# Kernel tuning notes

Measured on AMD Instinct MI355X. Metric: run time of the kernel, lower is better.

The kernel has to match this reference:

```python
import jax, jax.numpy as jnp
import numpy as np

EMBED, HEADS, LEVELS, POINTS = 256, 8, 4, 4
SPATIAL_SHAPES = np.array([[128, 128], [64, 64], [32, 32], [16, 16]], dtype=np.int32)


def _grid_init_bias():
    # Faithful reproduction of the sampling_offsets bias init (per-head directional grid).
    thetas = np.arange(HEADS, dtype=np.float32) * (2.0 * np.pi / HEADS)
    g = np.stack([np.cos(thetas), np.sin(thetas)], -1)
    g = g / np.abs(g).max(-1, keepdims=True)
    g = np.tile(g.reshape(HEADS, 1, 1, 2), (1, LEVELS, POINTS, 1))
    for i in range(POINTS):
        g[:, :, i, :] *= i + 1
    return g.reshape(-1).astype(np.float32)


def setup_inputs() -> dict:
    key = jax.random.key(0)
    ks = jax.random.split(key, 8)
    bs = 2
    V = int((SPATIAL_SHAPES[:, 0] * SPATIAL_SHAPES[:, 1]).sum())  # 21760
    Q = V  # encoder self-attention
    C = EMBED
    n_off = HEADS * LEVELS * POINTS * 2
    n_attn = HEADS * LEVELS * POINTS
    inv_sqrt_c = 1.0 / np.sqrt(C)
    return {
        "query": jax.random.normal(ks[0], (bs, Q, C), jnp.float32),
        "value": jax.random.normal(ks[1], (bs, V, C), jnp.float32),
        "reference_points": jax.random.uniform(ks[2], (bs, Q, LEVELS, 2), jnp.float32),
        "spatial_shapes": SPATIAL_SHAPES,  # static int array
        # learned parameters (torch Linear stored as [in, out]: y = x @ W + b)
        "W_off": jax.random.normal(ks[3], (C, n_off), jnp.float32) * 0.01,
        "b_off": jnp.asarray(_grid_init_bias()),
        "W_attn": jax.random.normal(ks[4], (C, n_attn), jnp.float32) * 0.02,
        "b_attn": jnp.zeros((n_attn,), jnp.float32),
        "W_v": jax.random.normal(ks[5], (C, C), jnp.float32) * inv_sqrt_c,
        "b_v": jnp.zeros((C,), jnp.float32),
        "W_out": jax.random.normal(ks[6], (C, C), jnp.float32) * inv_sqrt_c,
        "b_out": jnp.zeros((C,), jnp.float32),
    }


def _ms_deform_attn(query, value, reference_points, shapes,
                    W_off, b_off, W_attn, b_attn, W_v, b_v, W_out, b_out):
    bs, Q, C = query.shape
    d = C // HEADS
    # value projection -> [bs, heads, V, d]
    val = (value @ W_v + b_v).reshape(bs, -1, HEADS, d).transpose(0, 2, 1, 3)
    # sampling offsets and attention weights from query
    off = (query @ W_off + b_off).reshape(bs, Q, HEADS, LEVELS, POINTS, 2)
    attn = jax.nn.softmax(
        (query @ W_attn + b_attn).reshape(bs, Q, HEADS, LEVELS * POINTS), axis=-1
    ).reshape(bs, Q, HEADS, LEVELS, POINTS)
    # offset normalizer is (W, H) per level
    norm = jnp.asarray(np.stack([shapes[:, 1], shapes[:, 0]], -1), jnp.float32)  # [L,2]
    loc = reference_points[:, :, None, :, None, :] + off / norm[None, None, None, :, None, :]

    out = jnp.zeros((bs, HEADS, Q, d), query.dtype)
    start = 0
    for l in range(LEVELS):
        H, W = int(shapes[l, 0]), int(shapes[l, 1])
        v_l = val[:, :, start:start + H * W]  # [bs, heads, H*W, d]
        start += H * W
        loc_l = loc[:, :, :, l]    # [bs, Q, heads, P, 2] in [0,1]
        attn_l = attn[:, :, :, l]  # [bs, Q, heads, P]
        # grid_sample(align_corners=False, padding_mode='zeros') semantics
        g = 2.0 * loc_l - 1.0
        x = (g[..., 0] + 1.0) * 0.5 * W - 0.5
        y = (g[..., 1] + 1.0) * 0.5 * H - 0.5
        x0 = jnp.floor(x)
        y0 = jnp.floor(y)
        for dx in (0, 1):
            for dy in (0, 1):
                xi = x0 + dx
                yi = y0 + dy
                w = (1.0 - jnp.abs(x - xi)) * (1.0 - jnp.abs(y - yi))
                valid = (xi >= 0) & (xi <= W - 1) & (yi >= 0) & (yi <= H - 1)
                w = jnp.where(valid, w, 0.0) * attn_l  # fused corner + attention weight
                idx = (jnp.clip(yi, 0, H - 1).astype(jnp.int32) * W
                       + jnp.clip(xi, 0, W - 1).astype(jnp.int32))  # [bs,Q,heads,P]
                idx_t = jnp.transpose(idx, (0, 2, 1, 3)).reshape(bs, HEADS, Q * POINTS)
                vals = jnp.take_along_axis(v_l, idx_t[..., None], axis=2)
                vals = vals.reshape(bs, HEADS, Q, POINTS, d)
                out = out + jnp.einsum('bhqpd,bqhp->bhqd', vals, w)
    out = out.transpose(0, 2, 1, 3).reshape(bs, Q, C)  # heads-major channel layout
    return out @ W_out + b_out


def reference(query, value, reference_points, spatial_shapes,
              W_off, b_off, W_attn, b_attn, W_v, b_v, W_out, b_out):
    shapes = np.asarray(spatial_shapes)  # static
    return _ms_deform_attn(query, value, reference_points, shapes,
                           W_off, b_off, W_attn, b_attn, W_v, b_v, W_out, b_out)
```

## Files before the change

kernel.cpp:

```cpp
#include <hip/hip_runtime.h>
#include <math.h>

#define QN 21760
#define MTOT 43520
#define SZBQC 11141120

typedef __attribute__((ext_vector_type(8))) short bf16x8;
typedef __attribute__((ext_vector_type(4))) float f32x4;

__device__ inline ushort f2bf(float f) {
  union { float f; uint u; } v; v.f = f;
  return (ushort)((v.u + 0x7FFFu + ((v.u >> 16) & 1u)) >> 16);
}
__device__ inline uint pk2(float lo, float hi) { return (uint)f2bf(lo) | ((uint)f2bf(hi) << 16); }

__device__ inline void g2l(const ushort* g, ushort* l) {
  __builtin_amdgcn_global_load_lds(
      (const __attribute__((address_space(1))) void*)g,
      (__attribute__((address_space(3))) void*)l, 16, 0, 0);
}

__global__ __launch_bounds__(256) void prep_weights(
    const float* __restrict__ Wv, const float* __restrict__ Wout,
    const float* __restrict__ Woff, const float* __restrict__ Wattn,
    const float* __restrict__ boff, const float* __restrict__ battn,
    ushort* __restrict__ wv_t, ushort* __restrict__ wout_t,
    ushort* __restrict__ wol_t, float* __restrict__ biasf) {
  int bidx = blockIdx.x, t = threadIdx.x;
  if (bidx < 256) {
    int idx = bidx * 256 + t; int n = idx >> 8, k = idx & 255;
    wv_t[idx] = f2bf(Wv[(size_t)k * 256 + n]);
  } else if (bidx < 512) {
    int idx = (bidx - 256) * 256 + t; int n = idx >> 8, k = idx & 255;
    wout_t[idx] = f2bf(Wout[(size_t)k * 256 + n]);
  } else {
    int idx = (bidx - 512) * 256 + t; int n = idx >> 8, k = idx & 255;
    float v = (n < 256) ? Woff[(size_t)k * 256 + n] : Wattn[(size_t)k * 128 + (n - 256)];
    wol_t[idx] = f2bf(v);
    if (idx < 384) biasf[idx] = (idx < 256) ? boff[idx] : battn[idx - 256];
  }
}


__global__ __launch_bounds__(256) void gemm_in(
    const float* __restrict__ value, const float* __restrict__ query,
    const ushort* __restrict__ Wv, const ushort* __restrict__ Wol,
    const float* __restrict__ bv, const float* __restrict__ bol,
    ushort* __restrict__ val_out, float* __restrict__ offlog) {
  __shared__ ushort As[2][4096];
  __shared__ ushort Bs[2][4096];
  const int bid = blockIdx.x;
  const int q5  = bid >> 3;
  const int bxv = (bid & 7) + 8 * (q5 / 5);
  const int bx  = q5 % 5;
  if (bxv >= 340) return;
  const int t = threadIdx.x, wave = t >> 6, lane = t & 63;
  const int bm = bxv * 128;
  const bool isVal = bx < 2;
  const float* A   = isVal ? value : query;
  const ushort* Bt = isVal ? (Wv + (size_t)bx * 128 * 256)
                           : (Wol + (size_t)(bx - 2) * 128 * 256);
  const int wm = (wave >> 1) * 64, wn = (wave & 1) * 64;
  const int l15 = lane & 15, l4 = lane >> 4;
  const int pc = l4 ^ ((l15 >> 1) & 3);

  const int srow = lane >> 2;
  const int sch  = (lane & 3) ^ ((lane >> 3) & 3);
  const ushort* Bg = Bt + (size_t)(32 * wave + srow) * 256 + sch * 8;
  ushort* lb[2] = { &Bs[0][(32 * wave) * 32], &Bs[1][(32 * wave) * 32] };

  f32x4 acc[4][4];
#pragma unroll
  for (int i = 0; i < 4; ++i)
#pragma unroll
    for (int j = 0; j < 4; ++j) acc[i][j] = (f32x4){0.f, 0.f, 0.f, 0.f};

  int arow[4], apart[4];
#pragma unroll
  for (int i = 0; i < 4; ++i) {
    int c = t + i * 256; arow[i] = c >> 3; apart[i] = c & 7;
  }

  {
    float4 pa[4];
#pragma unroll
    for (int i = 0; i < 4; ++i)
      pa[i] = *(const float4*)&A[(size_t)(bm + arow[i]) * 256 + apart[i] * 4];
    g2l(Bg, lb[0]); g2l(Bg + 16 * 256, lb[0] + 16 * 32);
#pragma unroll
    for (int i = 0; i < 4; ++i) {
      int pc16 = (apart[i] >> 1) ^ ((arow[i] >> 1) & 3);
      ushort4 hv = { f2bf(pa[i].x), f2bf(pa[i].y), f2bf(pa[i].z), f2bf(pa[i].w) };
      *(ushort4*)&As[0][arow[i] * 32 + pc16 * 8 + (apart[i] & 1) * 4] = hv;
    }
  }

  for (int k = 0; k < 8; ++k) {
    __syncthreads();
    const int cur = k & 1, nxt = cur ^ 1;
    float4 pa[4];
    if (k < 7) {
      int k1 = (k + 1) * 32;
#pragma unroll
      for (int i = 0; i < 4; ++i)
        pa[i] = *(const float4*)&A[(size_t)(bm + arow[i]) * 256 + k1 + apart[i] * 4];
      g2l(Bg + k1, lb[nxt]); g2l(Bg + 16 * 256 + k1, lb[nxt] + 16 * 32);
    }
    bf16x8 af[4], bfr[4];
#pragma unroll
    for (int mi = 0; mi < 4; ++mi)
      af[mi] = *(const bf16x8*)&As[cur][(wm + mi * 16 + l15) * 32 + pc * 8];
#pragma unroll
    for (int ni = 0; ni < 4; ++ni)
      bfr[ni] = *(const bf16x8*)&Bs[cur][(wn + ni * 16 + l15) * 32 + pc * 8];
#pragma unroll
    for (int mi = 0; mi < 4; ++mi)
#pragma unroll
      for (int ni = 0; ni < 4; ++ni)
        acc[mi][ni] = __builtin_amdgcn_mfma_f32_16x16x32_bf16(af[mi], bfr[ni], acc[mi][ni], 0, 0, 0);
    if (k < 7) {
#pragma unroll
      for (int i = 0; i < 4; ++i) {
        int pc16 = (apart[i] >> 1) ^ ((arow[i] >> 1) & 3);
        ushort4 hv = { f2bf(pa[i].x), f2bf(pa[i].y), f2bf(pa[i].z), f2bf(pa[i].w) };
        *(ushort4*)&As[nxt][arow[i] * 32 + pc16 * 8 + (apart[i] & 1) * 4] = hv;
      }
    }
  }

  if (isVal) {
    _Float16* vo = (_Float16*)val_out;
#pragma unroll
    for (int mi = 0; mi < 4; ++mi)
#pragma unroll
      for (int ni = 0; ni < 4; ++ni) {
        int col = bx * 128 + wn + ni * 16 + l15;
        float bb = bv[col];
        int hh = col >> 5, c = col & 31;
#pragma unroll
        for (int r = 0; r < 4; ++r) {
          int row = bm + wm + mi * 16 + l4 * 4 + r;
          int b = (row >= QN) ? 1 : 0;
          int vpos = row - b * QN;
          vo[((size_t)(b * 8 + hh) * QN + vpos) * 32 + c] = (_Float16)(acc[mi][ni][r] + bb);
        }
      }
  } else {
#pragma unroll
    for (int mi = 0; mi < 4; ++mi)
#pragma unroll
      for (int ni = 0; ni < 4; ++ni) {
        int col = (bx - 2) * 128 + wn + ni * 16 + l15;
        float bb = bol[col];
#pragma unroll
        for (int r = 0; r < 4; ++r) {
          int row = bm + wm + mi * 16 + l4 * 4 + r;
          offlog[(size_t)row * 384 + col] = acc[mi][ni][r] + bb;
        }
      }
  }
}

__global__ __launch_bounds__(256) void gemm_out(
    const ushort* __restrict__ A, const ushort* __restrict__ Bt,
    const float* __restrict__ bias, float* __restrict__ C) {
  __shared__ ushort As[2][4096];
  __shared__ ushort Bs[2][4096];
  const int bid = blockIdx.x;
  const int q2  = bid >> 3;
  const int bxv = (bid & 7) + 8 * (q2 >> 1);
  const int byv = q2 & 1;
  if (bxv >= 340) return;
  const int t = threadIdx.x, wave = t >> 6, lane = t & 63;
  const int bm = bxv * 128, bn = byv * 128;
  const int wm = (wave >> 1) * 64, wn = (wave & 1) * 64;
  const int l15 = lane & 15, l4 = lane >> 4;
  const int pc = l4 ^ ((l15 >> 1) & 3);

  const int srow = lane >> 2;
  const int sch  = (lane & 3) ^ ((lane >> 3) & 3);
  const ushort* Ag = A + (size_t)(bm + 32 * wave + srow) * 256 + sch * 8;
  const ushort* Bg = Bt + (size_t)(bn + 32 * wave + srow) * 256 + sch * 8;
  ushort* la[2] = { &As[0][(32 * wave) * 32], &As[1][(32 * wave) * 32] };
  ushort* lb[2] = { &Bs[0][(32 * wave) * 32], &Bs[1][(32 * wave) * 32] };

  f32x4 acc[4][4];
#pragma unroll
  for (int i = 0; i < 4; ++i)
#pragma unroll
    for (int j = 0; j < 4; ++j) acc[i][j] = (f32x4){0.f, 0.f, 0.f, 0.f};

  g2l(Ag, la[0]); g2l(Ag + 16 * 256, la[0] + 16 * 32);
  g2l(Bg, lb[0]); g2l(Bg + 16 * 256, lb[0] + 16 * 32);

  for (int k = 0; k < 8; ++k) {
    __syncthreads();
    const int cur = k & 1, nxt = cur ^ 1;
    if (k < 7) {
      int k1 = (k + 1) * 32;
      g2l(Ag + k1, la[nxt]); g2l(Ag + 16 * 256 + k1, la[nxt] + 16 * 32);
      g2l(Bg + k1, lb[nxt]); g2l(Bg + 16 * 256 + k1, lb[nxt] + 16 * 32);
    }
    bf16x8 af[4], bfr[4];
#pragma unroll
    for (int mi = 0; mi < 4; ++mi)
      af[mi] = *(const bf16x8*)&As[cur][(wm + mi * 16 + l15) * 32 + pc * 8];
#pragma unroll
    for (int ni = 0; ni < 4; ++ni)
      bfr[ni] = *(const bf16x8*)&Bs[cur][(wn + ni * 16 + l15) * 32 + pc * 8];
#pragma unroll
    for (int mi = 0; mi < 4; ++mi)
#pragma unroll
      for (int ni = 0; ni < 4; ++ni)
        acc[mi][ni] = __builtin_amdgcn_mfma_f32_16x16x32_bf16(af[mi], bfr[ni], acc[mi][ni], 0, 0, 0);
  }

#pragma unroll
  for (int mi = 0; mi < 4; ++mi)
#pragma unroll
    for (int ni = 0; ni < 4; ++ni) {
      int col = bn + wn + ni * 16 + l15;
      float bb = bias[col];
#pragma unroll
      for (int r = 0; r < 4; ++r) {
        int row = bm + wm + mi * 16 + l4 * 4 + r;
        C[(size_t)row * 256 + col] = acc[mi][ni][r] + bb;
      }
    }
}

__device__ inline void fmah(float* a, uint4 u, float wv) {
  union { uint4 u; _Float16 h[8]; } c; c.u = u;
#pragma unroll
  for (int i = 0; i < 8; ++i) a[i] = fmaf((float)c.h[i], wv, a[i]);
}

__global__ __launch_bounds__(256) void msda_sample(
    const ushort* __restrict__ val, const float* __restrict__ offlog,
    const float* __restrict__ ref, ushort* __restrict__ interm) {
  int h   = blockIdx.x & 7;
  int z   = blockIdx.x >> 3;
  int sub = threadIdx.x & 3;
  int bq  = z * 64 + (threadIdx.x >> 2);
  int b   = (bq >= QN) ? 1 : 0;
  const uint sub8 = (uint)(sub * 8);
  const ushort* vb = val + (size_t)((uint)(b * 8 + h) * (uint)QN) * 32u + sub8;

  const float* lgp = offlog + (size_t)bq * 384 + 256 + h * 16;
  float4 lg = *(const float4*)(lgp + sub * 4);
  float m = fmaxf(fmaxf(lg.x, lg.y), fmaxf(lg.z, lg.w));
  m = fmaxf(m, __shfl_xor(m, 1, 64));
  m = fmaxf(m, __shfl_xor(m, 2, 64));
  float e0 = __expf(lg.x - m), e1 = __expf(lg.y - m),
        e2 = __expf(lg.z - m), e3 = __expf(lg.w - m);
  float s = e0 + e1 + e2 + e3;
  s += __shfl_xor(s, 1, 64);
  s += __shfl_xor(s, 2, 64);
  float inv = __builtin_amdgcn_rcpf(s);
  float aw[4] = { e0 * inv, e1 * inv, e2 * inv, e3 * inv };

  const int  Wl  = 128 >> sub;
  const uint t16 = 65536u >> (sub + sub);
  const int  lst = (int)((65536u - t16) / 3u);
  const float fW = (float)Wl;
  const float* offp = offlog + (size_t)bq * 384 + h * 32;
  float4 o0 = *(const float4*)(offp + sub * 8);
  float4 o1 = *(const float4*)(offp + sub * 8 + 4);
  float2 rf = *(const float2*)(ref + (size_t)bq * 8 + sub * 2);
  const float xb = rf.x * fW - 0.5f;
  const float yb = rf.y * fW - 0.5f;
  float ox[4] = { o0.x, o0.z, o1.x, o1.z };
  float oy[4] = { o0.y, o0.w, o1.y, o1.w };

  uint  pA0[4], pA1[4], pDX[4];
  float pX0[4], pX1[4], pY0[4], pY1[4];
#pragma unroll
  for (int p = 0; p < 4; ++p) {
    float x = xb + ox[p], y = yb + oy[p];
    float x0f = floorf(x), y0f = floorf(y);
    float fx = x - x0f, fy = y - y0f;
    int x0 = (int)x0f, y0 = (int)y0f;
    float a = aw[p];
    pX0[p] = ((uint)x0       < (uint)Wl) ? (1.f - fx) : 0.f;
    pX1[p] = ((uint)(x0 + 1) < (uint)Wl) ? fx         : 0.f;
    pY0[p] = (((uint)y0       < (uint)Wl) ? (1.f - fy) : 0.f) * a;
    pY1[p] = (((uint)(y0 + 1) < (uint)Wl) ? fy         : 0.f) * a;
    int xc0 = min(max(x0, 0), Wl - 1);
    int xc1 = min(max(x0 + 1, 0), Wl - 1);
    int yc0 = min(max(y0, 0), Wl - 1);
    int yc1 = min(max(y0 + 1, 0), Wl - 1);
    pA0[p] = (uint)((lst + yc0 * Wl + xc0) * 32);
    pA1[p] = (uint)((lst + yc1 * Wl + xc0) * 32);
    pDX[p] = (uint)((xc1 - xc0) * 32);
  }

  float acc[8];
#pragma unroll
  for (int i = 0; i < 8; ++i) acc[i] = 0.f;

  const int lanebase = (threadIdx.x & 63) & 60;
#pragma unroll
  for (int l = 0; l < 4; ++l) {
    const int src = lanebase | l;
#pragma unroll
    for (int p = 0; p < 4; ++p) {
      uint  A0  = (uint)__shfl((int)pA0[p], src, 64);
      uint  A1  = (uint)__shfl((int)pA1[p], src, 64);
      uint  DX  = (uint)__shfl((int)pDX[p], src, 64);
      float wx0 = __shfl(pX0[p], src, 64);
      float wx1 = __shfl(pX1[p], src, 64);
      float wy0 = __shfl(pY0[p], src, 64);
      float wy1 = __shfl(pY1[p], src, 64);
      uint4 u00 = *(const uint4*)(vb + A0);
      uint4 u01 = *(const uint4*)(vb + A0 + DX);
      uint4 u10 = *(const uint4*)(vb + A1);
      uint4 u11 = *(const uint4*)(vb + A1 + DX);
      fmah(acc, u00, wx0 * wy0);
      fmah(acc, u01, wx1 * wy0);
      fmah(acc, u10, wx0 * wy1);
      fmah(acc, u11, wx1 * wy1);
    }
  }

  uint4 o;
  o.x = pk2(acc[0], acc[1]); o.y = pk2(acc[2], acc[3]);
  o.z = pk2(acc[4], acc[5]); o.w = pk2(acc[6], acc[7]);
  *(uint4*)(interm + (size_t)bq * 256 + h * 32 + sub * 8) = o;
}

extern "C" void kernel_launch(void* const* d_in, const int* in_sizes, int n_in,
                              void* d_out, int out_size, void* d_ws, size_t ws_size,
                              hipStream_t stream) {
  const float* query = (const float*)d_in[0];
  const float* value = (const float*)d_in[1];
  const float* ref   = (const float*)d_in[2];
  const float* W_off  = (const float*)d_in[4];
  const float* b_off  = (const float*)d_in[5];
  const float* W_attn = (const float*)d_in[6];
  const float* b_attn = (const float*)d_in[7];
  const float* W_v    = (const float*)d_in[8];
  const float* b_v    = (const float*)d_in[9];
  const float* W_out  = (const float*)d_in[10];
  const float* b_out  = (const float*)d_in[11];
  float* out = (float*)d_out;

  char* wsb = (char*)d_ws;
  ushort* ws_wv     = (ushort*)(wsb + 0);
  ushort* ws_wol    = (ushort*)(wsb + 131072);
  ushort* ws_wout   = (ushort*)(wsb + 327680);
  float*  ws_biasf  = (float*)(wsb + 458752);
  ushort* ws_val    = (ushort*)(wsb + 462848);
  ushort* ws_interm = (ushort*)(wsb + 22745088);
  float*  ws_offlog = (float*)(wsb + 45027328);
  size_t need = (size_t)45027328 + 66846720;
  if (ws_size < need) return;

  dim3 blk(256);
  prep_weights<<<dim3(896), blk, 0, stream>>>(W_v, W_out, W_off, W_attn, b_off, b_attn,
                                              ws_wv, ws_wout, ws_wol, ws_biasf);
  gemm_in<<<dim3(1720), blk, 0, stream>>>(value, query, ws_wv, ws_wol, b_v, ws_biasf,
                                          ws_val, ws_offlog);
  msda_sample<<<dim3(5440), blk, 0, stream>>>(ws_val, ws_offlog, ref, ws_interm);
  gemm_out<<<dim3(688), blk, 0, stream>>>(ws_interm, ws_wout, b_out, out);
}
```

Before: 277.3 us.

## Split bilinear x-corners across lanes and pipeline gathers in deformable sampling

```diff
diff --git a/kernel.cpp b/kernel.cpp
--- a/kernel.cpp
+++ b/kernel.cpp
@@ -49,13 +49,8 @@
     ushort* __restrict__ val_out, float* __restrict__ offlog) {
   __shared__ ushort As[2][4096];
   __shared__ ushort Bs[2][4096];
-  const int bid = blockIdx.x;
-  const int q5  = bid >> 3;
-  const int bxv = (bid & 7) + 8 * (q5 / 5);
-  const int bx  = q5 % 5;
-  if (bxv >= 340) return;
   const int t = threadIdx.x, wave = t >> 6, lane = t & 63;
-  const int bm = bxv * 128;
+  const int bx = blockIdx.y, bm = blockIdx.x * 128;
   const bool isVal = bx < 2;
   const float* A   = isVal ? value : query;
   const ushort* Bt = isVal ? (Wv + (size_t)bx * 128 * 256)
@@ -166,13 +161,8 @@
     const float* __restrict__ bias, float* __restrict__ C) {
   __shared__ ushort As[2][4096];
   __shared__ ushort Bs[2][4096];
-  const int bid = blockIdx.x;
-  const int q2  = bid >> 3;
-  const int bxv = (bid & 7) + 8 * (q2 >> 1);
-  const int byv = q2 & 1;
-  if (bxv >= 340) return;
   const int t = threadIdx.x, wave = t >> 6, lane = t & 63;
-  const int bm = bxv * 128, bn = byv * 128;
+  const int bm = blockIdx.x * 128, bn = blockIdx.y * 128;
   const int wm = (wave >> 1) * 64, wn = (wave & 1) * 64;
   const int l15 = lane & 15, l4 = lane >> 4;
   const int pc = l4 ^ ((l15 >> 1) & 3);
@@ -240,40 +230,41 @@
     const float* __restrict__ ref, ushort* __restrict__ interm) {
   int h   = blockIdx.x & 7;
   int z   = blockIdx.x >> 3;
-  int sub = threadIdx.x & 3;
-  int bq  = z * 64 + (threadIdx.x >> 2);
+  int s   = threadIdx.x & 7;
+  int o   = s & 3;
+  bool xs = s >= 4;
+  int bq  = z * 32 + (threadIdx.x >> 3);
   int b   = (bq >= QN) ? 1 : 0;
-  const uint sub8 = (uint)(sub * 8);
-  const ushort* vb = val + (size_t)((uint)(b * 8 + h) * (uint)QN) * 32u + sub8;
+  const ushort* vbl = val + (size_t)((uint)(b * 8 + h) * (uint)QN) * 32u + (uint)(s * 8);
 
   const float* lgp = offlog + (size_t)bq * 384 + 256 + h * 16;
-  float4 lg = *(const float4*)(lgp + sub * 4);
+  float4 lg = *(const float4*)(lgp + o * 4);
   float m = fmaxf(fmaxf(lg.x, lg.y), fmaxf(lg.z, lg.w));
   m = fmaxf(m, __shfl_xor(m, 1, 64));
   m = fmaxf(m, __shfl_xor(m, 2, 64));
   float e0 = __expf(lg.x - m), e1 = __expf(lg.y - m),
         e2 = __expf(lg.z - m), e3 = __expf(lg.w - m);
-  float s = e0 + e1 + e2 + e3;
-  s += __shfl_xor(s, 1, 64);
-  s += __shfl_xor(s, 2, 64);
-  float inv = __builtin_amdgcn_rcpf(s);
+  float ssum = e0 + e1 + e2 + e3;
+  ssum += __shfl_xor(ssum, 1, 64);
+  ssum += __shfl_xor(ssum, 2, 64);
+  float inv = __builtin_amdgcn_rcpf(ssum);
   float aw[4] = { e0 * inv, e1 * inv, e2 * inv, e3 * inv };
 
-  const int  Wl  = 128 >> sub;
-  const uint t16 = 65536u >> (sub + sub);
+  const int  Wl  = 128 >> o;
+  const uint t16 = 65536u >> (o + o);
   const int  lst = (int)((65536u - t16) / 3u);
   const float fW = (float)Wl;
   const float* offp = offlog + (size_t)bq * 384 + h * 32;
-  float4 o0 = *(const float4*)(offp + sub * 8);
-  float4 o1 = *(const float4*)(offp + sub * 8 + 4);
-  float2 rf = *(const float2*)(ref + (size_t)bq * 8 + sub * 2);
+  float4 f0 = *(const float4*)(offp + o * 8);
+  float4 f1 = *(const float4*)(offp + o * 8 + 4);
+  float2 rf = *(const float2*)(ref + (size_t)bq * 8 + o * 2);
   const float xb = rf.x * fW - 0.5f;
   const float yb = rf.y * fW - 0.5f;
-  float ox[4] = { o0.x, o0.z, o1.x, o1.z };
-  float oy[4] = { o0.y, o0.w, o1.y, o1.w };
-
-  uint  pA0[4], pA1[4], pDX[4];
-  float pX0[4], pX1[4], pY0[4], pY1[4];
+  float ox[4] = { f0.x, f0.z, f1.x, f1.z };
+  float oy[4] = { f0.y, f0.w, f1.y, f1.w };
+
+  uint  pA0[4], pA1[4];
+  float pW0[4], pW1[4], pY0[4], pY1[4];
 #pragma unroll
   for (int p = 0; p < 4; ++p) {
     float x = xb + ox[p], y = yb + oy[p];
@@ -281,51 +272,66 @@
     float fx = x - x0f, fy = y - y0f;
     int x0 = (int)x0f, y0 = (int)y0f;
     float a = aw[p];
-    pX0[p] = ((uint)x0       < (uint)Wl) ? (1.f - fx) : 0.f;
-    pX1[p] = ((uint)(x0 + 1) < (uint)Wl) ? fx         : 0.f;
+    float wx0 = ((uint)x0       < (uint)Wl) ? (1.f - fx) : 0.f;
+    float wx1 = ((uint)(x0 + 1) < (uint)Wl) ? fx         : 0.f;
     pY0[p] = (((uint)y0       < (uint)Wl) ? (1.f - fy) : 0.f) * a;
     pY1[p] = (((uint)(y0 + 1) < (uint)Wl) ? fy         : 0.f) * a;
     int xc0 = min(max(x0, 0), Wl - 1);
     int xc1 = min(max(x0 + 1, 0), Wl - 1);
     int yc0 = min(max(y0, 0), Wl - 1);
     int yc1 = min(max(y0 + 1, 0), Wl - 1);
-    pA0[p] = (uint)((lst + yc0 * Wl + xc0) * 32);
-    pA1[p] = (uint)((lst + yc1 * Wl + xc0) * 32);
-    pDX[p] = (uint)((xc1 - xc0) * 32);
+    int xbase = min(max(x0, 0), Wl - 2);
+    pW0[p] = ((xbase     == xc0) ? wx0 : 0.f) + ((xbase     == xc1) ? wx1 : 0.f);
+    pW1[p] = ((xbase + 1 == xc0) ? wx0 : 0.f) + ((xbase + 1 == xc1) ? wx1 : 0.f);
+    pA0[p] = (uint)((lst + yc0 * Wl + xbase) * 32);
+    pA1[p] = (uint)((lst + yc1 * Wl + xbase) * 32);
   }
 
   float acc[8];
 #pragma unroll
   for (int i = 0; i < 8; ++i) acc[i] = 0.f;
 
-  const int lanebase = (threadIdx.x & 63) & 60;
-#pragma unroll
-  for (int l = 0; l < 4; ++l) {
-    const int src = lanebase | l;
-#pragma unroll
-    for (int p = 0; p < 4; ++p) {
-      uint  A0  = (uint)__shfl((int)pA0[p], src, 64);
-      uint  A1  = (uint)__shfl((int)pA1[p], src, 64);
-      uint  DX  = (uint)__shfl((int)pDX[p], src, 64);
-      float wx0 = __shfl(pX0[p], src, 64);
-      float wx1 = __shfl(pX1[p], src, 64);
-      float wy0 = __shfl(pY0[p], src, 64);
-      float wy1 = __shfl(pY1[p], src, 64);
-      uint4 u00 = *(const uint4*)(vb + A0);
-      uint4 u01 = *(const uint4*)(vb + A0 + DX);
-      uint4 u10 = *(const uint4*)(vb + A1);
-      uint4 u11 = *(const uint4*)(vb + A1 + DX);
-      fmah(acc, u00, wx0 * wy0);
-      fmah(acc, u01, wx1 * wy0);
-      fmah(acc, u10, wx0 * wy1);
-      fmah(acc, u11, wx1 * wy1);
-    }
-  }
-
-  uint4 o;
-  o.x = pk2(acc[0], acc[1]); o.y = pk2(acc[2], acc[3]);
-  o.z = pk2(acc[4], acc[5]); o.w = pk2(acc[6], acc[7]);
-  *(uint4*)(interm + (size_t)bq * 256 + h * 32 + sub * 8) = o;
+  const int gb = (threadIdx.x & 63) & ~7;
+
+  uint  bA0[2], bA1[2];
+  float bW[2], bY0[2], bY1[2];
+  uint4 u0[2], u1[2];
+
+#define MSDA_BCAST(J, S) do {                                   \
+    const int l_ = (J) >> 2, p_ = (J) & 3;                      \
+    const int src_ = gb | l_;                                   \
+    bA0[S] = (uint)__shfl((int)pA0[p_], src_, 64);              \
+    bA1[S] = (uint)__shfl((int)pA1[p_], src_, 64);              \
+    float w0_ = __shfl(pW0[p_], src_, 64);                      \
+    float w1_ = __shfl(pW1[p_], src_, 64);                      \
+    bW[S]  = xs ? w1_ : w0_;                                    \
+    bY0[S] = __shfl(pY0[p_], src_, 64);                         \
+    bY1[S] = __shfl(pY1[p_], src_, 64);                         \
+  } while (0)
+#define MSDA_LOAD(S) do {                                       \
+    u0[S] = *(const uint4*)(vbl + bA0[S]);                      \
+    u1[S] = *(const uint4*)(vbl + bA1[S]);                      \
+  } while (0)
+
+  MSDA_BCAST(0, 0);
+  MSDA_LOAD(0);
+#pragma unroll
+  for (int j = 0; j < 16; ++j) {
+    const int cur = j & 1, nxt = cur ^ 1;
+    if (j < 15) { MSDA_BCAST(j + 1, nxt); MSDA_LOAD(nxt); }
+    fmah(acc, u0[cur], bW[cur] * bY0[cur]);
+    fmah(acc, u1[cur], bW[cur] * bY1[cur]);
+  }
+#undef MSDA_BCAST
+#undef MSDA_LOAD
+
+#pragma unroll
+  for (int i = 0; i < 8; ++i) acc[i] += __shfl_xor(acc[i], 4, 64);
+
+  uint2 ov;
+  if (!xs) { ov.x = pk2(acc[0], acc[1]); ov.y = pk2(acc[2], acc[3]); }
+  else     { ov.x = pk2(acc[4], acc[5]); ov.y = pk2(acc[6], acc[7]); }
+  *(uint2*)(interm + (size_t)bq * 256 + h * 32 + (s & 3) * 8 + (xs ? 4 : 0)) = ov;
 }
 
 extern "C" void kernel_launch(void* const* d_in, const int* in_sizes, int n_in,
@@ -358,8 +364,8 @@
   dim3 blk(256);
   prep_weights<<<dim3(896), blk, 0, stream>>>(W_v, W_out, W_off, W_attn, b_off, b_attn,
                                               ws_wv, ws_wout, ws_wol, ws_biasf);
-  gemm_in<<<dim3(1720), blk, 0, stream>>>(value, query, ws_wv, ws_wol, b_v, ws_biasf,
-                                          ws_val, ws_offlog);
-  msda_sample<<<dim3(5440), blk, 0, stream>>>(ws_val, ws_offlog, ref, ws_interm);
-  gemm_out<<<dim3(688), blk, 0, stream>>>(ws_interm, ws_wout, b_out, out);
-}
+  gemm_in<<<dim3(340, 5), blk, 0, stream>>>(value, query, ws_wv, ws_wol, b_v, ws_biasf,
+                                            ws_val, ws_offlog);
+  msda_sample<<<dim3(10880), blk, 0, stream>>>(ws_val, ws_offlog, ref, ws_interm);
+  gemm_out<<<dim3(340, 2), blk, 0, stream>>>(ws_interm, ws_wout, b_out, out);
+}
```

Result: faster. 267.7 us (-3.5%).
